# Optimization experiments

Measured on AMD Instinct MI355X. Metric: run time of the kernel, lower is better.

## Reference

```python
import jax, jax.numpy as jnp
import numpy as np

N_NODES = 200000
N_EDGES = 800000
D_IN = 64
D_OUT = 64
NUM_RELATIONS = 16
NUM_BASES = 8


def setup_inputs() -> dict:
    key = jax.random.key(0)
    k_x, k_s, k_t, k_r, k_b, k_a = jax.random.split(key, 6)
    x = jax.random.normal(k_x, (N_NODES, D_IN), dtype=jnp.float32)
    node_keep_mask = jnp.ones((N_NODES,), dtype=bool)
    source = jax.random.randint(k_s, (N_EDGES,), 0, N_NODES, dtype=jnp.int64)
    target = jax.random.randint(k_t, (N_EDGES,), 0, N_NODES, dtype=jnp.int64)
    edge_type = jax.random.randint(k_r, (N_EDGES,), 0, NUM_RELATIONS, dtype=jnp.int64)
    # parameters: xavier-normal bases, L1-normalized attention coefficients
    std = float(np.sqrt(2.0 / (D_IN + D_OUT)))
    bases = jax.random.normal(k_b, (NUM_BASES, D_IN, D_OUT), dtype=jnp.float32) * std
    att = jax.random.uniform(k_a, (NUM_RELATIONS + 1, NUM_BASES), dtype=jnp.float32)
    att = att / jnp.sum(jnp.abs(att), axis=1, keepdims=True)
    return {"x": x, "node_keep_mask": node_keep_mask, "source": source,
            "target": target, "edge_type": edge_type, "bases": bases, "att": att}


def reference(x, node_keep_mask, source, target, edge_type, bases, att):
    num_relations = att.shape[0] - 1
    # per-node, per-basis transformed features: (N, B, D_out)
    t = jnp.einsum('nd,bde->nbe', x, bases)
    # self-loop term (att row num_relations), masked by node_keep_mask
    self_msg = jnp.einsum('nbe,b->ne', t, att[num_relations])
    out = jnp.where(node_keep_mask[:, None], self_msg, jnp.zeros((), dtype=x.dtype))
    # per-node, per-relation messages: (N, R, D_out) -- collapses the per-relation
    # python loop of the original into one contraction
    h = jnp.einsum('nbe,rb->nre', t, att[:num_relations])
    # bidirectional edges (original concatenates [src,tgt] and [tgt,src])
    src2 = jnp.concatenate([source, target])
    tgt2 = jnp.concatenate([target, source])
    et2 = jnp.concatenate([edge_type, edge_type])
    m = h[src2, et2]  # (2E, D_out) gather
    out = out.at[tgt2].add(m)  # scatter-add over edges
    return out
```

## Files before the change

kernel.cpp:

```cpp
#include <hip/hip_runtime.h>
#include <hip/hip_bf16.h>
#include <stdint.h>
#include <stddef.h>

#define N_NODES 200000
#define N_EDGES 800000
#define NREL 16
#define NBASES 8

typedef __attribute__((ext_vector_type(8))) short short8b;
typedef __attribute__((ext_vector_type(4))) float float4v;
typedef __attribute__((ext_vector_type(4))) int int4v;

__device__ __forceinline__ short f32_bf16(float f) {
  uint32_t u = __builtin_bit_cast(uint32_t, f);
  uint32_t r = u + 0x7FFFu + ((u >> 16) & 1u);
  return (short)(uint16_t)(r >> 16);
}
__device__ __forceinline__ uint16_t f32_bf16_hw(float f) {
  __hip_bfloat16 h = __float2bfloat16(f);
  return __builtin_bit_cast(uint16_t, h);
}
__device__ __forceinline__ float bf2f(uint16_t h) {
  return __builtin_bit_cast(float, (uint32_t)h << 16);
}

__global__ __launch_bounds__(256) void k_wprep(const float* __restrict__ bases,
                                               const float* __restrict__ att,
                                               uint16_t* __restrict__ Wt) {
  int i = blockIdx.x * 256 + threadIdx.x;
  if (i >= 17 * 64 * 64) return;
  int r = i >> 12;
  int e = (i >> 6) & 63;
  int d = i & 63;
  float acc = 0.f;
  for (int b = 0; b < NBASES; ++b)
    acc += att[r * NBASES + b] * bases[b * 4096 + d * 64 + e];
  Wt[i] = (uint16_t)f32_bf16(acc);
}

#define MAXTILES 112528
#define MAXRECS  (MAXTILES * 16)
#define WS_CNTR    0
#define WS_RCUR    128
#define WS_RSTART  256
#define WS_GCUR    384
#define WS_WT      512
#define WS_TILEREL 139776
#define WS_CNTV    252416
#define WS_VSTART  1052416
#define WS_CNTT    1852416
#define WS_RECS    2652416
#define WS_MSG     17056128
#define WS_TOTAL   (WS_MSG + (size_t)MAXRECS * 128)
#define OFF_EOFF   WS_MSG
#define OFF_NOFF   (WS_MSG + (size_t)N_EDGES*16)

__global__ __launch_bounds__(256) void k_init(const float* __restrict__ bases,
                                              const float* __restrict__ att,
                                              uint16_t* __restrict__ Wt,
                                              int* __restrict__ zero0,
                                              int* __restrict__ cntv) {
  int b = blockIdx.x;
  int tid = threadIdx.x;
  if (b < 273) {
    int i = b * 256 + tid;
    if (i < 17 * 64 * 64) {
      int r = i >> 12;
      int e = (i >> 6) & 63;
      int d = i & 63;
      float acc = 0.f;
      for (int bb = 0; bb < NBASES; ++bb)
        acc += att[r * NBASES + bb] * bases[bb * 4096 + d * 64 + e];
      Wt[i] = (uint16_t)f32_bf16(acc);
    }
  } else {
    int idx = (b - 273) * 256 + tid;
    if (idx < 128) zero0[idx] = 0;
    else if (idx - 128 < N_NODES) cntv[idx - 128] = 0;
  }
}

#define CNT_BLOCKS  782
#define CAST_BLOCKS 6250
__global__ __launch_bounds__(256) void k_count(const int* __restrict__ src,
                                               const int* __restrict__ tgt,
                                               const int* __restrict__ et,
                                               const int* __restrict__ mask,
                                               int* __restrict__ cntr,
                                               int* __restrict__ cntv,
                                               int4* __restrict__ eoff,
                                               int* __restrict__ noff,
                                               const float* __restrict__ x,
                                               uint16_t* __restrict__ xb,
                                               int nE, int nN) {
  int b = blockIdx.x;
  if (b >= CNT_BLOCKS) {
    int i = (b - CNT_BLOCKS) * 256 + threadIdx.x;
    const float* xp = x + (size_t)i * 8;
    float4v q0 = __builtin_nontemporal_load((const float4v*)xp);
    float4v q1 = __builtin_nontemporal_load((const float4v*)(xp + 4));
    short8b o;
    o[0] = f32_bf16_hw(q0[0]); o[1] = f32_bf16_hw(q0[1]); o[2] = f32_bf16_hw(q0[2]); o[3] = f32_bf16_hw(q0[3]);
    o[4] = f32_bf16_hw(q1[0]); o[5] = f32_bf16_hw(q1[1]); o[6] = f32_bf16_hw(q1[2]); o[7] = f32_bf16_hw(q1[3]);
    *(short8b*)(xb + (size_t)i * 8) = o;
    return;
  }
  __shared__ int lh[NREL + 1], lbase[NREL + 1];
  if (threadIdx.x <= NREL) lh[threadIdx.x] = 0;
  __syncthreads();
  int base = b * 1024 + threadIdx.x;
  bool isE[4], isN[4];
  int r4[4], loff[4], loffN[4], s4[4], t4[4];
#pragma unroll
  for (int k = 0; k < 4; ++k) {
    int i = base + k * 256;
    isE[k] = i < nE;
    isN[k] = (i < nN) && mask[i];
    if (isE[k]) {
      r4[k] = et[i];
      s4[k] = src[i];
      t4[k] = tgt[i];
      loff[k] = atomicAdd(&lh[r4[k]], 2);
    }
    if (isN[k]) loffN[k] = atomicAdd(&lh[NREL], 1);
  }
  __syncthreads();
  if (threadIdx.x <= NREL)
    lbase[threadIdx.x] = lh[threadIdx.x] ? atomicAdd(&cntr[threadIdx.x], lh[threadIdx.x]) : 0;
  __syncthreads();
  int o1[4], o2[4];
#pragma unroll
  for (int k = 0; k < 4; ++k) {
    if (isE[k]) {
      o1[k] = atomicAdd(&cntv[t4[k]], 1);
      o2[k] = atomicAdd(&cntv[s4[k]], 1);
    }
  }
#pragma unroll
  for (int k = 0; k < 4; ++k) {
    int i = base + k * 256;
    if (isE[k]) {
      int4v v; v[0] = lbase[r4[k]] + loff[k]; v[1] = o1[k]; v[2] = o2[k]; v[3] = 0;
      __builtin_nontemporal_store(v, (int4v*)(eoff + i));
    }
    if (isN[k]) __builtin_nontemporal_store(lbase[NREL] + loffN[k], noff + i);
  }
}

#define PREP_BLOCKS 440
#define VSEG_BLOCKS 782
__global__ __launch_bounds__(256) void k_scan(const int* __restrict__ cntr,
                                              int* __restrict__ rstart_g,
                                              uint8_t* __restrict__ tileRel,
                                              int2* __restrict__ recs,
                                              const int* __restrict__ cntv,
                                              const int* __restrict__ mask,
                                              int* __restrict__ vstart,
                                              int* __restrict__ cntt,
                                              int* __restrict__ gcur,
                                              int maxTiles, int nN) {
  int b = blockIdx.x;
  if (b < PREP_BLOCKS) {
    __shared__ int s[NREL + 2];
    if (threadIdx.x == 0) {
      int base = 0;
      for (int r = 0; r <= NREL; ++r) {
        s[r] = base;
        base = (base + cntr[r] + 15) & ~15;
      }
      s[NREL + 1] = base;
    }
    __syncthreads();
    if (b == 0) {
      if (threadIdx.x <= NREL + 1) rstart_g[threadIdx.x] = s[threadIdx.x];
      for (int w = threadIdx.x; w < (NREL + 1) * 16; w += 256) {
        int r = w >> 4, j = w & 15;
        int pos = s[r] + cntr[r] + j;
        if (pos < s[r + 1]) recs[pos] = make_int2(-1, -1);
      }
    }
    int t = b * 256 + threadIdx.x;
    if (t < maxTiles) {
      int p = t * 16;
      uint8_t rr = 255;
      if (p < s[NREL + 1]) {
        int q = 0;
        for (int k = 1; k <= NREL; ++k)
          if (p >= s[k]) q = k;
        rr = (uint8_t)q;
      }
      tileRel[t] = rr;
    }
  } else {
    __shared__ int wsum[4];
    __shared__ int s_base;
    int v = (b - PREP_BLOCKS) * 256 + threadIdx.x;
    int lane = threadIdx.x & 63;
    int wid = threadIdx.x >> 6;
    int c = 0;
    if (v < nN) c = cntv[v] + (mask[v] ? 1 : 0);
    int incl = c;
    for (int off = 1; off < 64; off <<= 1) {
      int n = __shfl_up(incl, off, 64);
      if (lane >= off) incl += n;
    }
    if (lane == 63) wsum[wid] = incl;
    __syncthreads();
    if (threadIdx.x == 0) {
      int t0 = wsum[0], t1 = wsum[1], t2 = wsum[2], t3 = wsum[3];
      s_base = atomicAdd(gcur, t0 + t1 + t2 + t3);
      wsum[0] = 0;
      wsum[1] = t0;
      wsum[2] = t0 + t1;
      wsum[3] = t0 + t1 + t2;
    }
    __syncthreads();
    if (v < nN) {
      vstart[v] = s_base + wsum[wid] + incl - c;
      cntt[v] = c;
    }
  }
}

__global__ __launch_bounds__(256) void k_write(const int* __restrict__ src,
                                               const int* __restrict__ tgt,
                                               const int* __restrict__ et,
                                               const int* __restrict__ mask,
                                               const int4* __restrict__ eoff,
                                               const int* __restrict__ noff,
                                               const int* __restrict__ rstart,
                                               const int* __restrict__ cntv,
                                               const int* __restrict__ vstart,
                                               int2* __restrict__ recs,
                                               int nE, int nN) {
  __shared__ int s_rs[NREL + 1];
  if (threadIdx.x <= NREL) s_rs[threadIdx.x] = rstart[threadIdx.x];
  __syncthreads();
  int i = blockIdx.x * 256 + threadIdx.x;
  if (i < nE) {
    int r = et[i];
    int4v e = __builtin_nontemporal_load((const int4v*)(eoff + i));
    int s_ = src[i], t_ = tgt[i];
    int pos = s_rs[r] + e[0];
    int s1 = vstart[t_] + e[1];
    int s2 = vstart[s_] + e[2];
    *(int4*)(recs + pos) = make_int4(s_, s1, t_, s2);
  }
  if (i < nN && mask[i]) {
    int pos = s_rs[NREL] + noff[i];
    int slot = vstart[i] + cntv[i];
    recs[pos] = make_int2(i, slot);
  }
}

__global__ __launch_bounds__(256) void k_phaseA(const uint16_t* __restrict__ xb,
                                                const int2* __restrict__ recs,
                                                const uint16_t* __restrict__ Wt,
                                                const uint8_t* __restrict__ tileRel,
                                                uint16_t* __restrict__ msg,
                                                int ntiles) {
  __shared__ uint16_t s_m[4][16 * 72];
  __shared__ int s_slot[4][16];
  const int wid = threadIdx.x >> 6;
  const int lane = threadIdx.x & 63;
  const int quad = lane >> 4;
  const int m16 = lane & 15;
  const int t0 = (blockIdx.x * 4 + wid) * 4;

  if (tileRel[t0] == 255) return;

  int rel4[4];
#pragma unroll
  for (int it = 0; it < 4; ++it) {
    int t = t0 + it;
    rel4[it] = (t < ntiles) ? (int)tileRel[t] : 255;
  }
  int2 rec4[4];
#pragma unroll
  for (int it = 0; it < 4; ++it) {
    if (rel4[it] != 255) {
      long long rv = __builtin_nontemporal_load((const long long*)(recs + (t0 + it) * 16 + m16));
      rec4[it].x = (int)(rv & 0xFFFFFFFFll);
      rec4[it].y = (int)(rv >> 32);
    } else {
      rec4[it] = make_int2(-1, -1);
    }
  }
  short8b a0_[4], a1_[4];
#pragma unroll
  for (int it = 0; it < 4; ++it) {
    int u = rec4[it].x < 0 ? 0 : rec4[it].x;
    const uint16_t* xp = xb + (size_t)u * 64 + quad * 8;
    a0_[it] = *(const short8b*)(xp);
    a1_[it] = *(const short8b*)(xp + 32);
  }

  int curRel = -1;
  short8b bfrag[4][2] = {};

#pragma unroll
  for (int it = 0; it < 4; ++it) {
    int rel = rel4[it];
    if (rel == 255) continue;

    if (rel != curRel) {
      curRel = rel;
      const uint16_t* wbase = Wt + (size_t)rel * 4096;
      for (int nt = 0; nt < 4; ++nt)
        for (int kt = 0; kt < 2; ++kt)
          bfrag[nt][kt] = *(const short8b*)(wbase + (size_t)(nt * 16 + m16) * 64 + kt * 32 + quad * 8);
    }

    float4v acc[4];
    for (int nt = 0; nt < 4; ++nt) { acc[nt][0] = 0.f; acc[nt][1] = 0.f; acc[nt][2] = 0.f; acc[nt][3] = 0.f; }
    for (int nt = 0; nt < 4; ++nt) {
      acc[nt] = __builtin_amdgcn_mfma_f32_16x16x32_bf16(a0_[it], bfrag[nt][0], acc[nt], 0, 0, 0);
      acc[nt] = __builtin_amdgcn_mfma_f32_16x16x32_bf16(a1_[it], bfrag[nt][1], acc[nt], 0, 0, 0);
    }

    if (quad == 0) s_slot[wid][m16] = rec4[it].y;
    for (int reg = 0; reg < 4; ++reg)
      for (int nt = 0; nt < 4; ++nt)
        s_m[wid][(quad * 4 + reg) * 72 + nt * 16 + m16] = f32_bf16_hw(acc[nt][reg]);

    asm volatile("s_waitcnt lgkmcnt(0)" ::: "memory");
    __builtin_amdgcn_sched_barrier(0);

    for (int p = 0; p < 2; ++p) {
      int row = (lane >> 3) + p * 8;
      int slot = s_slot[wid][row];
      if (slot >= 0) {
        const uint16_t* lp = &s_m[wid][row * 72 + (lane & 7) * 8];
        int4v val = *(const int4v*)lp;
        __builtin_nontemporal_store(val, (int4v*)(msg + (size_t)slot * 64 + (lane & 7) * 8));
      }
    }
    __builtin_amdgcn_sched_barrier(0);
  }
}

__global__ __launch_bounds__(256) void k_phaseB(const uint16_t* __restrict__ msg,
                                                const int* __restrict__ cntt,
                                                const int* __restrict__ vstart,
                                                float* __restrict__ out, int nN) {
  int v = blockIdx.x * 32 + (threadIdx.x >> 3);
  int l = threadIdx.x & 7;
  if (v >= nN) return;
  int cnt = cntt[v];
  int base = vstart[v];
  float a[8] = {0.f, 0.f, 0.f, 0.f, 0.f, 0.f, 0.f, 0.f};
  const uint16_t* mp = msg + (size_t)base * 64 + l * 8;
  int j = 0;
  for (; j + 2 <= cnt; j += 2) {
    int4v r0 = __builtin_nontemporal_load((const int4v*)(mp + (size_t)j * 64));
    int4v r1 = __builtin_nontemporal_load((const int4v*)(mp + (size_t)(j + 1) * 64));
    short8b h0 = __builtin_bit_cast(short8b, r0);
    short8b h1 = __builtin_bit_cast(short8b, r1);
#pragma unroll
    for (int k = 0; k < 8; ++k)
      a[k] += bf2f((uint16_t)h0[k]) + bf2f((uint16_t)h1[k]);
  }
  if (j < cnt) {
    int4v r0 = __builtin_nontemporal_load((const int4v*)(mp + (size_t)j * 64));
    short8b h = __builtin_bit_cast(short8b, r0);
#pragma unroll
    for (int k = 0; k < 8; ++k)
      a[k] += bf2f((uint16_t)h[k]);
  }
  float* op = out + (size_t)v * 64 + l * 8;
  float4v o0, o1;
  o0[0] = a[0]; o0[1] = a[1]; o0[2] = a[2]; o0[3] = a[3];
  o1[0] = a[4]; o1[1] = a[5]; o1[2] = a[6]; o1[3] = a[7];
  __builtin_nontemporal_store(o0, (float4v*)op);
  __builtin_nontemporal_store(o1, (float4v*)(op + 4));
}

#define F_WS_HIST    0
#define F_WS_CURSOR  64
#define F_WS_START   128
#define F_WS_WT      512
#define F_WS_TILEREL 139776
#define F_WS_RECS    262144
#define F_MAXTILES   112520
#define F_MAXRECS    (F_MAXTILES * 16)

__global__ __launch_bounds__(256) void f_hist(const int* __restrict__ et,
                                              int* __restrict__ hist, int nE) {
  __shared__ int lh[NREL];
  if (threadIdx.x < NREL) lh[threadIdx.x] = 0;
  __syncthreads();
  int i = blockIdx.x * 256 + threadIdx.x;
  if (i < nE) atomicAdd(&lh[et[i]], 2);
  __syncthreads();
  if (threadIdx.x < NREL && lh[threadIdx.x] > 0)
    atomicAdd(&hist[threadIdx.x], lh[threadIdx.x]);
}

__global__ __launch_bounds__(256) void f_prefix(const int* __restrict__ hist,
                                                int* __restrict__ cursor,
                                                int* __restrict__ start,
                                                uint8_t* __restrict__ tileRel,
                                                int nN, int maxTiles) {
  __shared__ int s_start[17];
  if (threadIdx.x == 0) {
    int base = nN;
    for (int r = 0; r < NREL; ++r) {
      s_start[r] = base;
      cursor[r] = base;
      start[r] = base;
      base = (base + hist[r] + 15) & ~15;
    }
    s_start[16] = base;
    start[16] = base;
  }
  __syncthreads();
  int endp = s_start[16];
  for (int t = threadIdx.x; t < maxTiles; t += 256) {
    int p = t * 16;
    uint8_t r;
    if (p < nN) r = 16;
    else if (p >= endp) r = 255;
    else {
      int q = 0;
      for (int k = 1; k < NREL; ++k) if (p >= s_start[k]) q = k;
      r = (uint8_t)q;
    }
    tileRel[t] = r;
  }
}

__global__ __launch_bounds__(256) void f_scatter(const int* __restrict__ src,
                                                 const int* __restrict__ tgt,
                                                 const int* __restrict__ et,
                                                 const int* __restrict__ mask,
                                                 int2* __restrict__ recs,
                                                 int* __restrict__ cursor,
                                                 int nE, int nN) {
  __shared__ int lh[NREL];
  __shared__ int lbase[NREL];
  if (threadIdx.x < NREL) lh[threadIdx.x] = 0;
  __syncthreads();
  int i = blockIdx.x * 256 + threadIdx.x;
  int r = 0, loff = 0;
  bool isEdge = (i < nE);
  if (isEdge) {
    r = et[i];
    loff = atomicAdd(&lh[r], 2);
  }
  __syncthreads();
  if (threadIdx.x < NREL)
    lbase[threadIdx.x] = (lh[threadIdx.x] > 0) ? atomicAdd(&cursor[threadIdx.x], lh[threadIdx.x]) : 0;
  __syncthreads();
  if (isEdge) {
    int pos = lbase[r] + loff;
    int s = src[i], t = tgt[i];
    *(int4*)(recs + pos) = make_int4(s, t, t, s);
  }
  if (i < nN) {
    recs[i] = (mask[i] != 0) ? make_int2(i, i) : make_int2(-1, -1);
  }
}

__global__ __launch_bounds__(256) void f_compute(const float* __restrict__ x,
                                                 const int2* __restrict__ recs,
                                                 const uint16_t* __restrict__ Wt,
                                                 const uint8_t* __restrict__ tileRel,
                                                 float* __restrict__ out,
                                                 int ntiles) {
  const int lane = threadIdx.x & 63;
  const int quad = lane >> 4;
  const int m16 = lane & 15;
  const int wave = blockIdx.x * 4 + (threadIdx.x >> 6);
  const int t0 = wave * 4;

  int curRel = -1;
  short8b bfrag[4][2] = {};

  for (int it = 0; it < 4; ++it) {
    int t = t0 + it;
    if (t >= ntiles) return;
    int rel = tileRel[t];
    if (rel == 255) return;

    if (rel != curRel) {
      curRel = rel;
      const uint16_t* wbase = Wt + (size_t)rel * 4096;
      for (int nt = 0; nt < 4; ++nt)
        for (int kt = 0; kt < 2; ++kt)
          bfrag[nt][kt] = *(const short8b*)(wbase + (size_t)(nt * 16 + m16) * 64 + kt * 32 + quad * 8);
    }

    int2 rec = recs[t * 16 + m16];
    int u = rec.x < 0 ? 0 : rec.x;

    const float* xp = x + (size_t)u * 64 + quad * 8;
    float4v q0 = *(const float4v*)(xp);
    float4v q1 = *(const float4v*)(xp + 4);
    float4v q2 = *(const float4v*)(xp + 32);
    float4v q3 = *(const float4v*)(xp + 36);
    short8b a0, a1;
    a0[0] = f32_bf16(q0[0]); a0[1] = f32_bf16(q0[1]); a0[2] = f32_bf16(q0[2]); a0[3] = f32_bf16(q0[3]);
    a0[4] = f32_bf16(q1[0]); a0[5] = f32_bf16(q1[1]); a0[6] = f32_bf16(q1[2]); a0[7] = f32_bf16(q1[3]);
    a1[0] = f32_bf16(q2[0]); a1[1] = f32_bf16(q2[1]); a1[2] = f32_bf16(q2[2]); a1[3] = f32_bf16(q2[3]);
    a1[4] = f32_bf16(q3[0]); a1[5] = f32_bf16(q3[1]); a1[6] = f32_bf16(q3[2]); a1[7] = f32_bf16(q3[3]);

    float4v acc[4];
    for (int nt = 0; nt < 4; ++nt) { acc[nt][0] = 0.f; acc[nt][1] = 0.f; acc[nt][2] = 0.f; acc[nt][3] = 0.f; }
    for (int nt = 0; nt < 4; ++nt) {
      acc[nt] = __builtin_amdgcn_mfma_f32_16x16x32_bf16(a0, bfrag[nt][0], acc[nt], 0, 0, 0);
      acc[nt] = __builtin_amdgcn_mfma_f32_16x16x32_bf16(a1, bfrag[nt][1], acc[nt], 0, 0, 0);
    }

    int tg[4];
    for (int reg = 0; reg < 4; ++reg)
      tg[reg] = __shfl(rec.y, quad * 4 + reg, 64);
    for (int reg = 0; reg < 4; ++reg) {
      if (tg[reg] < 0) continue;
      float* op = out + (size_t)tg[reg] * 64 + m16;
      for (int nt = 0; nt < 4; ++nt)
        __hip_atomic_fetch_add(op + nt * 16, acc[nt][reg], __ATOMIC_RELAXED, __HIP_MEMORY_SCOPE_AGENT);
    }
  }
}

extern "C" void kernel_launch(void* const* d_in, const int* in_sizes, int n_in,
                              void* d_out, int out_size, void* d_ws, size_t ws_size,
                              hipStream_t stream) {
  const float* x     = (const float*)d_in[0];
  const int*   mask  = (const int*)d_in[1];
  const int*   src   = (const int*)d_in[2];
  const int*   tgt   = (const int*)d_in[3];
  const int*   et    = (const int*)d_in[4];
  const float* bases = (const float*)d_in[5];
  const float* att   = (const float*)d_in[6];
  float* out = (float*)d_out;
  char* ws = (char*)d_ws;

  if (ws_size >= WS_TOTAL) {
    int*      cntr    = (int*)(ws + WS_CNTR);
    int*      rstart  = (int*)(ws + WS_RSTART);
    int*      gcur    = (int*)(ws + WS_GCUR);
    uint16_t* Wt      = (uint16_t*)(ws + WS_WT);
    uint8_t*  tileRel = (uint8_t*)(ws + WS_TILEREL);
    int*      cntv    = (int*)(ws + WS_CNTV);
    int*      vstart  = (int*)(ws + WS_VSTART);
    int*      cntt    = (int*)(ws + WS_CNTT);
    int2*     recs    = (int2*)(ws + WS_RECS);
    uint16_t* msg     = (uint16_t*)(ws + WS_MSG);
    int4*     eoff    = (int4*)(ws + OFF_EOFF);
    int*      noff    = (int*)(ws + OFF_NOFF);
    uint16_t* xb      = (uint16_t*)out;

    k_init<<<1055, 256, 0, stream>>>(bases, att, Wt, (int*)ws, cntv);
    k_count<<<CNT_BLOCKS + CAST_BLOCKS, 256, 0, stream>>>(src, tgt, et, mask, cntr, cntv, eoff, noff, x, xb, N_EDGES, N_NODES);
    k_scan<<<PREP_BLOCKS + VSEG_BLOCKS, 256, 0, stream>>>(cntr, rstart, tileRel, recs, cntv, mask, vstart, cntt, gcur, MAXTILES, N_NODES);
    k_write<<<(N_EDGES + 255) / 256, 256, 0, stream>>>(src, tgt, et, mask, eoff, noff, rstart, cntv, vstart, recs, N_EDGES, N_NODES);
    k_phaseA<<<(MAXTILES + 15) / 16, 256, 0, stream>>>(xb, recs, Wt, tileRel, msg, MAXTILES);
    k_phaseB<<<(N_NODES + 31) / 32, 256, 0, stream>>>(msg, cntt, vstart, out, N_NODES);
  } else {
    int*      hist    = (int*)(ws + F_WS_HIST);
    int*      cursor  = (int*)(ws + F_WS_CURSOR);
    int*      start   = (int*)(ws + F_WS_START);
    uint16_t* Wt      = (uint16_t*)(ws + F_WS_WT);
    uint8_t*  tileRel = (uint8_t*)(ws + F_WS_TILEREL);
    int2*     recs    = (int2*)(ws + F_WS_RECS);

    (void)hipMemsetAsync(out, 0, (size_t)N_NODES * 64 * sizeof(float), stream);
    (void)hipMemsetAsync(ws, 0, 512, stream);
    (void)hipMemsetAsync(recs, 0xFF, (size_t)F_MAXRECS * sizeof(int2), stream);

    k_wprep<<<(17 * 64 * 64 + 255) / 256, 256, 0, stream>>>(bases, att, Wt);
    f_hist<<<(N_EDGES + 255) / 256, 256, 0, stream>>>(et, hist, N_EDGES);
    f_prefix<<<1, 256, 0, stream>>>(hist, cursor, start, tileRel, N_NODES, F_MAXTILES);
    f_scatter<<<(N_EDGES + 255) / 256, 256, 0, stream>>>(src, tgt, et, mask, recs, cursor, N_EDGES, N_NODES);
    f_compute<<<(F_MAXTILES + 15) / 16, 256, 0, stream>>>(x, recs, Wt, tileRel, out, F_MAXTILES);
  }
}
```

Baseline: 340.4 us.

## Replace global per-node atomic counting with two-level bucketed counting sort

Instead of 1.6M global atomicAdds on per-node counters to assign each edge endpoint a slot, endpoints are first bucketed into 1024-node regions through per-block histograms, a prefix-scan kernel, and a scatter into region-ordered scratch. A per-region kernel then assigns slots with shared-memory atomics and writes the per-node counts. The aim is to remove contended, random global atomics, at the cost of three extra kernel launches and additional scratch traffic.

```diff
diff --git a/kernel.cpp b/kernel.cpp
--- a/kernel.cpp
+++ b/kernel.cpp
@@ -41,8 +41,11 @@
 
 #define MAXTILES 112528
 #define MAXRECS  (MAXTILES * 16)
+#define NB 196
+#define CNT_BLOCKS  782
+#define CAST_BLOCKS 6250
 #define WS_CNTR    0
-#define WS_RCUR    128
+#define WS_GCUR2   128
 #define WS_RSTART  256
 #define WS_GCUR    384
 #define WS_WT      512
@@ -53,14 +56,18 @@
 #define WS_RECS    2652416
 #define WS_MSG     17056128
 #define WS_TOTAL   (WS_MSG + (size_t)MAXRECS * 128)
-#define OFF_EOFF   WS_MSG
-#define OFF_NOFF   (WS_MSG + (size_t)N_EDGES*16)
+#define TR_RELOFF  WS_MSG
+#define TR_NOFF    (TR_RELOFF + 3200000)
+#define TR_ESLOT   (TR_NOFF + 800000)
+#define TR_SCRATCH (TR_ESLOT + 6400000)
+#define TR_H       (TR_SCRATCH + 6400000)
+#define TR_BASE    (TR_H + 613088)
+#define TR_REGS    (TR_BASE + 613088)
 
 __global__ __launch_bounds__(256) void k_init(const float* __restrict__ bases,
                                               const float* __restrict__ att,
                                               uint16_t* __restrict__ Wt,
-                                              int* __restrict__ zero0,
-                                              int* __restrict__ cntv) {
+                                              int* __restrict__ zero0) {
   int b = blockIdx.x;
   int tid = threadIdx.x;
   if (b < 273) {
@@ -75,28 +82,25 @@
       Wt[i] = (uint16_t)f32_bf16(acc);
     }
   } else {
-    int idx = (b - 273) * 256 + tid;
-    if (idx < 128) zero0[idx] = 0;
-    else if (idx - 128 < N_NODES) cntv[idx - 128] = 0;
-  }
-}
-
-#define CNT_BLOCKS  782
-#define CAST_BLOCKS 6250
+    if (tid < 128) zero0[tid] = 0;
+  }
+}
+
 __global__ __launch_bounds__(256) void k_count(const int* __restrict__ src,
                                                const int* __restrict__ tgt,
                                                const int* __restrict__ et,
                                                const int* __restrict__ mask,
                                                int* __restrict__ cntr,
-                                               int* __restrict__ cntv,
-                                               int4* __restrict__ eoff,
+                                               int* __restrict__ H,
+                                               int* __restrict__ reloff,
                                                int* __restrict__ noff,
                                                const float* __restrict__ x,
                                                uint16_t* __restrict__ xb,
                                                int nE, int nN) {
   int b = blockIdx.x;
+  int tid = threadIdx.x;
   if (b >= CNT_BLOCKS) {
-    int i = (b - CNT_BLOCKS) * 256 + threadIdx.x;
+    int i = (b - CNT_BLOCKS) * 256 + tid;
     const float* xp = x + (size_t)i * 8;
     float4v q0 = __builtin_nontemporal_load((const float4v*)xp);
     float4v q1 = __builtin_nontemporal_load((const float4v*)(xp + 4));
@@ -107,11 +111,13 @@
     return;
   }
   __shared__ int lh[NREL + 1], lbase[NREL + 1];
-  if (threadIdx.x <= NREL) lh[threadIdx.x] = 0;
-  __syncthreads();
-  int base = b * 1024 + threadIdx.x;
+  __shared__ int bh[NB];
+  if (tid <= NREL) lh[tid] = 0;
+  if (tid < NB) bh[tid] = 0;
+  __syncthreads();
+  int base = b * 1024 + tid;
   bool isE[4], isN[4];
-  int r4[4], loff[4], loffN[4], s4[4], t4[4];
+  int r4[4], loff[4], loffN[4];
 #pragma unroll
   for (int k = 0; k < 4; ++k) {
     int i = base + k * 256;
@@ -119,32 +125,119 @@
     isN[k] = (i < nN) && mask[i];
     if (isE[k]) {
       r4[k] = et[i];
-      s4[k] = src[i];
-      t4[k] = tgt[i];
+      int s_ = src[i], t_ = tgt[i];
       loff[k] = atomicAdd(&lh[r4[k]], 2);
+      atomicAdd(&bh[t_ >> 10], 1);
+      atomicAdd(&bh[s_ >> 10], 1);
     }
     if (isN[k]) loffN[k] = atomicAdd(&lh[NREL], 1);
   }
   __syncthreads();
-  if (threadIdx.x <= NREL)
-    lbase[threadIdx.x] = lh[threadIdx.x] ? atomicAdd(&cntr[threadIdx.x], lh[threadIdx.x]) : 0;
-  __syncthreads();
-  int o1[4], o2[4];
-#pragma unroll
-  for (int k = 0; k < 4; ++k) {
-    if (isE[k]) {
-      o1[k] = atomicAdd(&cntv[t4[k]], 1);
-      o2[k] = atomicAdd(&cntv[s4[k]], 1);
-    }
-  }
+  if (tid <= NREL)
+    lbase[tid] = lh[tid] ? atomicAdd(&cntr[tid], lh[tid]) : 0;
+  if (tid < NB) H[b * NB + tid] = bh[tid];
+  __syncthreads();
 #pragma unroll
   for (int k = 0; k < 4; ++k) {
     int i = base + k * 256;
-    if (isE[k]) {
-      int4v v; v[0] = lbase[r4[k]] + loff[k]; v[1] = o1[k]; v[2] = o2[k]; v[3] = 0;
-      __builtin_nontemporal_store(v, (int4v*)(eoff + i));
-    }
+    if (isE[k]) __builtin_nontemporal_store(lbase[r4[k]] + loff[k], reloff + i);
     if (isN[k]) __builtin_nontemporal_store(lbase[NREL] + loffN[k], noff + i);
+  }
+}
+
+__global__ __launch_bounds__(256) void k_base(const int* __restrict__ H,
+                                              int* __restrict__ baseM,
+                                              int* __restrict__ regStart,
+                                              int* __restrict__ regTot,
+                                              int* __restrict__ gcur2) {
+  int b = blockIdx.x;
+  int tid = threadIdx.x;
+  int lane = tid & 63, wid = tid >> 6;
+  int vals[4]; int ts = 0;
+#pragma unroll
+  for (int k = 0; k < 4; ++k) {
+    int idx = tid * 4 + k;
+    vals[k] = (idx < CNT_BLOCKS) ? H[idx * NB + b] : 0;
+    ts += vals[k];
+  }
+  int incl = ts;
+  for (int off = 1; off < 64; off <<= 1) {
+    int n = __shfl_up(incl, off, 64);
+    if (lane >= off) incl += n;
+  }
+  __shared__ int wsum[4];
+  __shared__ int s_start;
+  if (lane == 63) wsum[wid] = incl;
+  __syncthreads();
+  if (tid == 0) {
+    int t0 = wsum[0], t1 = wsum[1], t2 = wsum[2], t3 = wsum[3];
+    int tot = t0 + t1 + t2 + t3;
+    int st = atomicAdd(gcur2, tot);
+    regStart[b] = st;
+    regTot[b] = tot;
+    s_start = st;
+    wsum[0] = 0; wsum[1] = t0; wsum[2] = t0 + t1; wsum[3] = t0 + t1 + t2;
+  }
+  __syncthreads();
+  int run = s_start + wsum[wid] + incl - ts;
+#pragma unroll
+  for (int k = 0; k < 4; ++k) {
+    int idx = tid * 4 + k;
+    if (idx < CNT_BLOCKS) {
+      baseM[idx * NB + b] = run;
+      run += vals[k];
+    }
+  }
+}
+
+__global__ __launch_bounds__(256) void k_scat(const int* __restrict__ src,
+                                              const int* __restrict__ tgt,
+                                              const int* __restrict__ baseM,
+                                              int* __restrict__ scratch,
+                                              int nE) {
+  int b = blockIdx.x;
+  int tid = threadIdx.x;
+  __shared__ int bh[NB];
+  __shared__ int bb[NB];
+  if (tid < NB) { bh[tid] = 0; bb[tid] = baseM[b * NB + tid]; }
+  __syncthreads();
+#pragma unroll
+  for (int k = 0; k < 4; ++k) {
+    int i = b * 1024 + k * 256 + tid;
+    if (i < nE) {
+      int t_ = tgt[i], s_ = src[i];
+      int offT = atomicAdd(&bh[t_ >> 10], 1);
+      scratch[bb[t_ >> 10] + offT] = ((t_ & 1023) << 21) | (2 * i);
+      int offS = atomicAdd(&bh[s_ >> 10], 1);
+      scratch[bb[s_ >> 10] + offS] = ((s_ & 1023) << 21) | (2 * i + 1);
+    }
+  }
+}
+
+__global__ __launch_bounds__(256) void k_slot(const int* __restrict__ scratch,
+                                              const int* __restrict__ regStart,
+                                              const int* __restrict__ regTot,
+                                              int* __restrict__ eslot,
+                                              int* __restrict__ cntv,
+                                              int nN) {
+  int b = blockIdx.x;
+  int tid = threadIdx.x;
+  __shared__ int cnt[1024];
+#pragma unroll
+  for (int k = 0; k < 4; ++k) cnt[tid + k * 256] = 0;
+  __syncthreads();
+  int start = regStart[b];
+  int tot = regTot[b];
+  for (int it = tid; it < tot; it += 256) {
+    int rec = scratch[start + it];
+    int off = atomicAdd(&cnt[rec >> 21], 1);
+    eslot[rec & 0x1FFFFF] = off;
+  }
+  __syncthreads();
+#pragma unroll
+  for (int k = 0; k < 4; ++k) {
+    int v = b * 1024 + k * 256 + tid;
+    if (v < nN) cntv[v] = cnt[k * 256 + tid];
   }
 }
 
@@ -227,8 +320,9 @@
                                                const int* __restrict__ tgt,
                                                const int* __restrict__ et,
                                                const int* __restrict__ mask,
-                                               const int4* __restrict__ eoff,
+                                               const int* __restrict__ reloff,
                                                const int* __restrict__ noff,
+                                               const int* __restrict__ eslot,
                                                const int* __restrict__ rstart,
                                                const int* __restrict__ cntv,
                                                const int* __restrict__ vstart,
@@ -240,11 +334,14 @@
   int i = blockIdx.x * 256 + threadIdx.x;
   if (i < nE) {
     int r = et[i];
-    int4v e = __builtin_nontemporal_load((const int4v*)(eoff + i));
+    int rl = __builtin_nontemporal_load(reloff + i);
+    long long ev = __builtin_nontemporal_load((const long long*)(eslot + 2 * i));
+    int o1 = (int)(ev & 0xFFFFFFFFll);
+    int o2 = (int)(ev >> 32);
     int s_ = src[i], t_ = tgt[i];
-    int pos = s_rs[r] + e[0];
-    int s1 = vstart[t_] + e[1];
-    int s2 = vstart[s_] + e[2];
+    int pos = s_rs[r] + rl;
+    int s1 = vstart[t_] + o1;
+    int s2 = vstart[s_] + o2;
     *(int4*)(recs + pos) = make_int4(s_, s1, t_, s2);
   }
   if (i < nN && mask[i]) {
@@ -539,6 +636,7 @@
 
   if (ws_size >= WS_TOTAL) {
     int*      cntr    = (int*)(ws + WS_CNTR);
+    int*      gcur2   = (int*)(ws + WS_GCUR2);
     int*      rstart  = (int*)(ws + WS_RSTART);
     int*      gcur    = (int*)(ws + WS_GCUR);
     uint16_t* Wt      = (uint16_t*)(ws + WS_WT);
@@ -548,14 +646,23 @@
     int*      cntt    = (int*)(ws + WS_CNTT);
     int2*     recs    = (int2*)(ws + WS_RECS);
     uint16_t* msg     = (uint16_t*)(ws + WS_MSG);
-    int4*     eoff    = (int4*)(ws + OFF_EOFF);
-    int*      noff    = (int*)(ws + OFF_NOFF);
+    int*      reloff  = (int*)(ws + TR_RELOFF);
+    int*      noff    = (int*)(ws + TR_NOFF);
+    int*      eslot   = (int*)(ws + TR_ESLOT);
+    int*      scratch = (int*)(ws + TR_SCRATCH);
+    int*      H       = (int*)(ws + TR_H);
+    int*      baseM   = (int*)(ws + TR_BASE);
+    int*      regStart= (int*)(ws + TR_REGS);
+    int*      regTot  = regStart + NB;
     uint16_t* xb      = (uint16_t*)out;
 
-    k_init<<<1055, 256, 0, stream>>>(bases, att, Wt, (int*)ws, cntv);
-    k_count<<<CNT_BLOCKS + CAST_BLOCKS, 256, 0, stream>>>(src, tgt, et, mask, cntr, cntv, eoff, noff, x, xb, N_EDGES, N_NODES);
+    k_init<<<274, 256, 0, stream>>>(bases, att, Wt, (int*)ws);
+    k_count<<<CNT_BLOCKS + CAST_BLOCKS, 256, 0, stream>>>(src, tgt, et, mask, cntr, H, reloff, noff, x, xb, N_EDGES, N_NODES);
+    k_base<<<NB, 256, 0, stream>>>(H, baseM, regStart, regTot, gcur2);
+    k_scat<<<CNT_BLOCKS, 256, 0, stream>>>(src, tgt, baseM, scratch, N_EDGES);
+    k_slot<<<NB, 256, 0, stream>>>(scratch, regStart, regTot, eslot, cntv, N_NODES);
     k_scan<<<PREP_BLOCKS + VSEG_BLOCKS, 256, 0, stream>>>(cntr, rstart, tileRel, recs, cntv, mask, vstart, cntt, gcur, MAXTILES, N_NODES);
-    k_write<<<(N_EDGES + 255) / 256, 256, 0, stream>>>(src, tgt, et, mask, eoff, noff, rstart, cntv, vstart, recs, N_EDGES, N_NODES);
+    k_write<<<(N_EDGES + 255) / 256, 256, 0, stream>>>(src, tgt, et, mask, reloff, noff, eslot, rstart, cntv, vstart, recs, N_EDGES, N_NODES);
     k_phaseA<<<(MAXTILES + 15) / 16, 256, 0, stream>>>(xb, recs, Wt, tileRel, msg, MAXTILES);
     k_phaseB<<<(N_NODES + 31) / 32, 256, 0, stream>>>(msg, cntt, vstart, out, N_NODES);
   } else {
```

After: 308.7 us. 1.1x faster.
